# Kernel tuning notes

Measured on AMD Instinct MI355X. Metric: run time of the kernel, lower is better.

## Reference

```python
import jax, jax.numpy as jnp
import numpy as np

B, C, H, W = 8, 256, 64, 64
CQK = C // 8  # 32


def setup_inputs() -> dict:
    key = jax.random.key(0)
    ks = jax.random.split(key, 7)
    s = 0.02
    return {
        "feat_map": jax.random.normal(ks[0], (B, C, H, W), dtype=jnp.float32),
        "w1": jax.random.normal(ks[1], (CQK, C), dtype=jnp.float32) * s,
        "b1": jnp.zeros((CQK,), dtype=jnp.float32),
        "w2": jax.random.normal(ks[2], (CQK, C), dtype=jnp.float32) * s,
        "b2": jnp.zeros((CQK,), dtype=jnp.float32),
        "w3": jax.random.normal(ks[3], (C, C), dtype=jnp.float32) * s,
        "b3": jnp.zeros((C,), dtype=jnp.float32),
        "gamma": jnp.zeros((1,), dtype=jnp.float32),
    }


def reference(feat_map, w1, b1, w2, b2, w3, b3, gamma):
    b, c, h, w = feat_map.shape
    n = h * w
    x = feat_map.reshape(b, c, n)  # [B, C, N]
    # 1x1 convs == per-pixel linear maps over channels
    q = jnp.einsum("oc,bcn->bno", w1, x) + b1  # [B, N, C//8]
    k = jnp.einsum("oc,bcn->bon", w2, x) + b2[None, :, None]  # [B, C//8, N]
    v = jnp.einsum("oc,bcn->bon", w3, x) + b3[None, :, None]  # [B, C, N]
    relation = jnp.einsum("bno,bom->bnm", q, k)  # [B, N, N]
    attn = jax.nn.softmax(relation, axis=-1)  # softmax over last dim
    # feat_refine = bmm(v, attn^T): out[:, :, i] = sum_j v[:, :, j] * attn[i, j]
    feat_refine = jnp.einsum("bcm,bnm->bcn", v, attn).reshape(b, c, h, w)
    scaled = gamma[0] * feat_refine
    return (feat_refine, scaled)
```

## Files before the change

kernel.cpp:

```cpp
#include <hip/hip_runtime.h>
#include <cmath>

#define NB 8
#define CC 256
#define NPIX 4096
#define QB 128
#define KVB 64
#define NT (NPIX / KVB)
#define LOG2E 1.4426950408889634f

typedef __attribute__((ext_vector_type(4))) float f32x4;
typedef __attribute__((ext_vector_type(16))) float f32x16;
typedef __attribute__((ext_vector_type(8))) short s16x8;
typedef __attribute__((ext_vector_type(4))) unsigned int u32x4;
typedef __attribute__((ext_vector_type(2))) unsigned int u32x2;

__device__ __forceinline__ unsigned short f2bf(float f) {
    union { float f; unsigned int u; } v; v.f = f;
    return (unsigned short)((v.u + 0x7FFFu + ((v.u >> 16) & 1u)) >> 16);
}

__device__ __forceinline__ unsigned int cvt_pk_bf16(float lo, float hi) {
    unsigned int r;
    asm("v_cvt_pk_bf16_f32 %0, %1, %2" : "=v"(r) : "v"(lo), "v"(hi));
    return r;
}

__device__ __forceinline__ float u2f(unsigned int u) {
    union { unsigned int u; float f; } v; v.u = u; return v.f;
}

__global__ __launch_bounds__(320) void proj_gemm_kernel(
    const float* __restrict__ x,
    const float* __restrict__ w1, const float* __restrict__ b1,
    const float* __restrict__ w2, const float* __restrict__ b2,
    const float* __restrict__ w3, const float* __restrict__ b3,
    unsigned short* __restrict__ Qm, unsigned short* __restrict__ Km,
    unsigned short* __restrict__ Vm)
{
    const int b  = blockIdx.x >> 6;
    const int n0 = (blockIdx.x & 63) * 64;
    const int wave = threadIdx.x >> 6;
    const int lane = threadIdx.x & 63;
    const int cl = lane & 15, g = lane >> 4;

    const float* arow[4];
#pragma unroll
    for (int ct = 0; ct < 4; ++ct) {
        const int row = wave * 64 + ct * 16 + cl;
        if (row < 32)       arow[ct] = w1 + (size_t)row * 256;
        else if (row < 64)  arow[ct] = w2 + (size_t)(row - 32) * 256;
        else                arow[ct] = w3 + (size_t)(row - 64) * 256;
    }

    const float* xb = x + (size_t)b * CC * NPIX + n0 + cl;

    f32x4 acc[4][4];
#pragma unroll
    for (int ct = 0; ct < 4; ++ct)
#pragma unroll
        for (int nt = 0; nt < 4; ++nt) acc[ct][nt] = (f32x4){0.f, 0.f, 0.f, 0.f};

    for (int ks = 0; ks < 8; ++ks) {
        const int c0 = ks * 32;
        s16x8 ah[4];
#pragma unroll
        for (int ct = 0; ct < 4; ++ct) {
            const float* ap = arow[ct] + c0 + g * 8;
            f32x4 a0 = *(const f32x4*)ap;
            f32x4 a1 = *(const f32x4*)(ap + 4);
            u32x4 u;
            u[0] = cvt_pk_bf16(a0[0], a0[1]); u[1] = cvt_pk_bf16(a0[2], a0[3]);
            u[2] = cvt_pk_bf16(a1[0], a1[1]); u[3] = cvt_pk_bf16(a1[2], a1[3]);
            ah[ct] = __builtin_bit_cast(s16x8, u);
        }
#pragma unroll
        for (int nt = 0; nt < 4; ++nt) {
            const float* xp = xb + (size_t)(c0 + g * 8) * NPIX + nt * 16;
            float xe[8];
#pragma unroll
            for (int e = 0; e < 8; ++e) xe[e] = xp[(size_t)e * NPIX];
            u32x4 uh, ul;
#pragma unroll
            for (int p = 0; p < 4; ++p) {
                const unsigned int hp = cvt_pk_bf16(xe[2 * p], xe[2 * p + 1]);
                const float h0 = u2f(hp << 16);
                const float h1 = u2f(hp & 0xffff0000u);
                uh[p] = hp;
                ul[p] = cvt_pk_bf16(xe[2 * p] - h0, xe[2 * p + 1] - h1);
            }
            const s16x8 bh = __builtin_bit_cast(s16x8, uh);
            const s16x8 bl = __builtin_bit_cast(s16x8, ul);
#pragma unroll
            for (int ct = 0; ct < 4; ++ct)
                acc[ct][nt] = __builtin_amdgcn_mfma_f32_16x16x32_bf16(ah[ct], bh, acc[ct][nt], 0, 0, 0);
#pragma unroll
            for (int ct = 0; ct < 4; ++ct)
                acc[ct][nt] = __builtin_amdgcn_mfma_f32_16x16x32_bf16(ah[ct], bl, acc[ct][nt], 0, 0, 0);
        }
    }

    if (wave == 0) {
#pragma unroll
        for (int ct = 0; ct < 4; ++ct) {
#pragma unroll
            for (int nt = 0; nt < 4; ++nt) {
                const int n = n0 + nt * 16 + cl;
                const int co = ct * 16 + g * 4;
                f32x4 v = acc[ct][nt];
                if (ct < 2) {
                    const float q0 = (v[0] + b1[co + 0]) * LOG2E;
                    const float q1 = (v[1] + b1[co + 1]) * LOG2E;
                    const float q2 = (v[2] + b1[co + 2]) * LOG2E;
                    const float q3 = (v[3] + b1[co + 3]) * LOG2E;
                    u32x2 dd = {cvt_pk_bf16(q0, q1), cvt_pk_bf16(q2, q3)};
                    *(u32x2*)(Qm + ((size_t)b * NPIX + n) * 32 + co) = dd;
                } else {
                    const int ko = co - 32;
                    const float k0 = v[0] + b2[ko + 0];
                    const float k1 = v[1] + b2[ko + 1];
                    const float k2 = v[2] + b2[ko + 2];
                    const float k3 = v[3] + b2[ko + 3];
                    u32x2 dd = {cvt_pk_bf16(k0, k1), cvt_pk_bf16(k2, k3)};
                    *(u32x2*)(Km + ((size_t)b * NPIX + n) * 32 + ko) = dd;
                }
            }
        }
    } else {
        const int cvb = (wave - 1) * 64;
#pragma unroll
        for (int ct = 0; ct < 4; ++ct) {
#pragma unroll
            for (int nt = 0; nt < 4; ++nt) {
                const int n = n0 + nt * 16 + cl;
                const int cv = cvb + ct * 16 + g * 4;
#pragma unroll
                for (int r = 0; r < 4; ++r)
                    Vm[((size_t)b * CC + cv + r) * NPIX + n] = f2bf(acc[ct][nt][r] + b3[cv + r]);
            }
        }
    }
}

__global__ __launch_bounds__(256, 2) void attn_kernel(
    const unsigned short* __restrict__ Qm, const unsigned short* __restrict__ Km,
    const unsigned short* __restrict__ Vm, const float* __restrict__ gamma,
    float* __restrict__ out)
{
    __shared__ unsigned short Vs[2][CC * KVB];

    const int bid = ((blockIdx.x & 7) << 5) + (blockIdx.x >> 3);
    const int b = bid >> 5;
    const int q0 = (bid & 31) * QB;

    const int t = threadIdx.x;
    const int wave = t >> 6;
    const int lane = t & 63;
    const int q_ = lane & 31;
    const int hi = lane >> 5;

    const int qrow = q0 + wave * 32 + q_;

    s16x8 qf[2];
#pragma unroll
    for (int kh = 0; kh < 2; ++kh)
        qf[kh] = *(const s16x8*)(Qm + ((size_t)b * NPIX + qrow) * 32 + kh * 16 + hi * 8);

    f32x16 acc[8];
#pragma unroll
    for (int ct = 0; ct < 8; ++ct) acc[ct] = (f32x16){};

    float mrun = -__builtin_inff();
    float lrun = 0.f;

    const unsigned short* Kg = Km + (size_t)b * NPIX * 32;
    const unsigned short* Vg = Vm + (size_t)b * CC * NPIX;

    const int vr0 = t >> 3;
    const int cg = (t & 7) ^ (vr0 & 7);
    const unsigned short* vsrc = Vg + (size_t)vr0 * NPIX + cg * 8;

#define STAGE_V(tile, buf_)                                                    \
    {                                                                          \
        const int mm_ = (tile) * KVB;                                          \
        _Pragma("unroll")                                                      \
        for (int i_ = 0; i_ < 8; ++i_)                                         \
            __builtin_amdgcn_global_load_lds(                                  \
                (const __attribute__((address_space(1))) void*)(vsrc + (size_t)i_ * 32 * NPIX + mm_), \
                (__attribute__((address_space(3))) void*)(&Vs[buf_][i_ * 2048 + t * 8]), \
                16, 0, 0);                                                     \
    }

    s16x8 kf[2][2];
#define LOAD_KF(mm_)                                                           \
    {                                                                          \
        _Pragma("unroll")                                                      \
        for (int mt_ = 0; mt_ < 2; ++mt_)                                      \
            _Pragma("unroll")                                                  \
            for (int kh_ = 0; kh_ < 2; ++kh_)                                  \
                kf[mt_][kh_] = *(const s16x8*)(Kg + (size_t)((mm_) + 32 * mt_ + q_) * 32 + kh_ * 16 + hi * 8); \
    }

    STAGE_V(0, 0)
    LOAD_KF(0)

    int cur = 0;
    for (int it = 0; it < NT; ++it) {
        __syncthreads();

        if (it < NT - 1) STAGE_V(it + 1, cur ^ 1)

        f32x16 z = (f32x16){};
        f32x16 s0 = __builtin_amdgcn_mfma_f32_32x32x16_bf16(kf[0][0], qf[0], z, 0, 0, 0);
        s0 = __builtin_amdgcn_mfma_f32_32x32x16_bf16(kf[0][1], qf[1], s0, 0, 0, 0);
        f32x16 s1 = __builtin_amdgcn_mfma_f32_32x32x16_bf16(kf[1][0], qf[0], z, 0, 0, 0);
        s1 = __builtin_amdgcn_mfma_f32_32x32x16_bf16(kf[1][1], qf[1], s1, 0, 0, 0);

        LOAD_KF((((it + 1) & (NT - 1))) * KVB)

        float ml = -__builtin_inff();
#pragma unroll
        for (int r = 0; r < 16; ++r) ml = fmaxf(ml, s0[r]);
#pragma unroll
        for (int r = 0; r < 16; ++r) ml = fmaxf(ml, s1[r]);

        if (!__all(ml <= mrun + 8.f)) {
            ml = fmaxf(ml, __shfl_xor(ml, 32, 64));
            const float mnew = fmaxf(mrun, ml);
            const float alpha = __builtin_amdgcn_exp2f(mrun - mnew);
            mrun = mnew;
            lrun *= alpha;
#pragma unroll
            for (int ct = 0; ct < 8; ++ct) acc[ct] *= alpha;
        }

#pragma unroll
        for (int r = 0; r < 16; ++r) { s0[r] = __builtin_amdgcn_exp2f(s0[r] - mrun); lrun += s0[r]; }
#pragma unroll
        for (int r = 0; r < 16; ++r) { s1[r] = __builtin_amdgcn_exp2f(s1[r] - mrun); lrun += s1[r]; }

        unsigned int w0[4][2], w1[4][2];
#pragma unroll
        for (int s = 0; s < 4; ++s) {
            w0[s][0] = cvt_pk_bf16(s0[4 * s + 0], s0[4 * s + 1]);
            w0[s][1] = cvt_pk_bf16(s0[4 * s + 2], s0[4 * s + 3]);
            w1[s][0] = cvt_pk_bf16(s1[4 * s + 0], s1[4 * s + 1]);
            w1[s][1] = cvt_pk_bf16(s1[4 * s + 2], s1[4 * s + 3]);
        }

#pragma unroll
        for (int t4 = 0; t4 < 4; ++t4) {
            const int lt = t4 & 1;
            unsigned int a0 = (t4 < 2) ? w0[2 * lt][0] : w1[2 * lt][0];
            unsigned int b0 = (t4 < 2) ? w0[2 * lt + 1][0] : w1[2 * lt + 1][0];
            unsigned int a1 = (t4 < 2) ? w0[2 * lt][1] : w1[2 * lt][1];
            unsigned int b1 = (t4 < 2) ? w0[2 * lt + 1][1] : w1[2 * lt + 1][1];
            asm("v_permlane32_swap_b32 %0, %1" : "+v"(a0), "+v"(b0));
            asm("v_permlane32_swap_b32 %0, %1" : "+v"(a1), "+v"(b1));
            u32x4 bw = {a0, a1, b0, b1};
            const s16x8 pb = __builtin_bit_cast(s16x8, bw);

            __builtin_amdgcn_s_setprio(1);
#pragma unroll
            for (int ct = 0; ct < 8; ++ct) {
                const int c = 32 * ct + q_;
                const int slot = (2 * t4 + hi) ^ (c & 7);
                const s16x8 av = *(const s16x8*)(&Vs[cur][c * 64 + slot * 8]);
                acc[ct] = __builtin_amdgcn_mfma_f32_32x32x16_bf16(av, pb, acc[ct], 0, 0, 0);
            }
            __builtin_amdgcn_s_setprio(0);
        }

        cur ^= 1;
    }

    lrun += __shfl_xor(lrun, 32, 64);
    const float inv = 1.f / lrun;
    const float gm = gamma[0];
    float* out2 = out + (size_t)NB * CC * NPIX;
    const int n = qrow;
#pragma unroll
    for (int ct = 0; ct < 8; ++ct) {
#pragma unroll
        for (int r = 0; r < 16; ++r) {
            const int c = 32 * ct + (r & 3) + 8 * (r >> 2) + 4 * hi;
            const float val = acc[ct][r] * inv;
            const size_t idx = ((size_t)b * CC + c) * NPIX + n;
            out[idx] = val;
            out2[idx] = gm * val;
        }
    }
}

extern "C" void kernel_launch(void* const* d_in, const int* in_sizes, int n_in,
                              void* d_out, int out_size, void* d_ws, size_t ws_size,
                              hipStream_t stream) {
    (void)in_sizes; (void)n_in; (void)out_size; (void)ws_size;
    const float* x     = (const float*)d_in[0];
    const float* w1    = (const float*)d_in[1];
    const float* b1    = (const float*)d_in[2];
    const float* w2    = (const float*)d_in[3];
    const float* b2    = (const float*)d_in[4];
    const float* w3    = (const float*)d_in[5];
    const float* b3    = (const float*)d_in[6];
    const float* gamma = (const float*)d_in[7];
    float* out = (float*)d_out;

    unsigned short* Qm = (unsigned short*)d_ws;
    unsigned short* Km = Qm + (size_t)NB * NPIX * 32;
    unsigned short* Vm = Km + (size_t)NB * NPIX * 32;

    proj_gemm_kernel<<<NB * 64, 320, 0, stream>>>(x, w1, b1, w2, b2, w3, b3, Qm, Km, Vm);
    attn_kernel<<<NB * 32, 256, 0, stream>>>(Qm, Km, Vm, gamma, out);
}
```

Before: 135.7 us.

## Split KV range across two wave groups per block and merge softmax partials

Doubles the attention block to 512 threads, with two groups of four waves each processing half of the key/value sequence using separate double-buffered V tiles in LDS. At the end, per-row max and sum are exchanged via shared memory and the second group's rescaled accumulators are staged through LDS to be combined by the first group. This aims to raise waves per CU and latency hiding, since the grid has only one block per CU. The cost is doubled LDS usage and an extra merge phase with barriers.

Measured after the change: 124.6 us. 1.09x faster.

```diff
diff --git a/kernel.cpp b/kernel.cpp
--- a/kernel.cpp
+++ b/kernel.cpp
@@ -6,7 +6,7 @@
 #define NPIX 4096
 #define QB 128
 #define KVB 64
-#define NT (NPIX / KVB)
+#define NT2 32
 #define LOG2E 1.4426950408889634f
 
 typedef __attribute__((ext_vector_type(4))) float f32x4;
@@ -142,12 +142,14 @@
     }
 }
 
-__global__ __launch_bounds__(256, 2) void attn_kernel(
+__global__ __launch_bounds__(512, 2) void attn_kernel(
     const unsigned short* __restrict__ Qm, const unsigned short* __restrict__ Km,
     const unsigned short* __restrict__ Vm, const float* __restrict__ gamma,
     float* __restrict__ out)
 {
-    __shared__ unsigned short Vs[2][CC * KVB];
+    __shared__ unsigned short Vs[2][2][CC * KVB];
+    __shared__ float mArr[2][4][32];
+    __shared__ float lArr[2][4][32];
 
     const int bid = ((blockIdx.x & 7) << 5) + (blockIdx.x >> 3);
     const int b = bid >> 5;
@@ -158,8 +160,10 @@
     const int lane = t & 63;
     const int q_ = lane & 31;
     const int hi = lane >> 5;
-
-    const int qrow = q0 + wave * 32 + q_;
+    const int s = wave & 3;
+    const int h = wave >> 2;
+
+    const int qrow = q0 + s * 32 + q_;
 
     s16x8 qf[2];
 #pragma unroll
@@ -176,18 +180,19 @@
     const unsigned short* Kg = Km + (size_t)b * NPIX * 32;
     const unsigned short* Vg = Vm + (size_t)b * CC * NPIX;
 
-    const int vr0 = t >> 3;
-    const int cg = (t & 7) ^ (vr0 & 7);
+    const int tg = t & 255;
+    const int vr0 = tg >> 3;
+    const int cg = (tg & 7) ^ (vr0 & 7);
     const unsigned short* vsrc = Vg + (size_t)vr0 * NPIX + cg * 8;
 
 #define STAGE_V(tile, buf_)                                                    \
     {                                                                          \
-        const int mm_ = (tile) * KVB;                                          \
+        const int mm_ = h * 2048 + (tile) * KVB;                               \
         _Pragma("unroll")                                                      \
         for (int i_ = 0; i_ < 8; ++i_)                                         \
             __builtin_amdgcn_global_load_lds(                                  \
                 (const __attribute__((address_space(1))) void*)(vsrc + (size_t)i_ * 32 * NPIX + mm_), \
-                (__attribute__((address_space(3))) void*)(&Vs[buf_][i_ * 2048 + t * 8]), \
+                (__attribute__((address_space(3))) void*)(&Vs[h][buf_][i_ * 2048 + tg * 8]), \
                 16, 0, 0);                                                     \
     }
 
@@ -202,13 +207,13 @@
     }
 
     STAGE_V(0, 0)
-    LOAD_KF(0)
+    LOAD_KF(h * 2048)
 
     int cur = 0;
-    for (int it = 0; it < NT; ++it) {
+    for (int it = 0; it < NT2; ++it) {
         __syncthreads();
 
-        if (it < NT - 1) STAGE_V(it + 1, cur ^ 1)
+        if (it < NT2 - 1) STAGE_V(it + 1, cur ^ 1)
 
         f32x16 z = (f32x16){};
         f32x16 s0 = __builtin_amdgcn_mfma_f32_32x32x16_bf16(kf[0][0], qf[0], z, 0, 0, 0);
@@ -216,7 +221,7 @@
         f32x16 s1 = __builtin_amdgcn_mfma_f32_32x32x16_bf16(kf[1][0], qf[0], z, 0, 0, 0);
         s1 = __builtin_amdgcn_mfma_f32_32x32x16_bf16(kf[1][1], qf[1], s1, 0, 0, 0);
 
-        LOAD_KF((((it + 1) & (NT - 1))) * KVB)
+        LOAD_KF(h * 2048 + (((it + 1) & (NT2 - 1))) * KVB)
 
         float ml = -__builtin_inff();
 #pragma unroll
@@ -241,11 +246,11 @@
 
         unsigned int w0[4][2], w1[4][2];
 #pragma unroll
-        for (int s = 0; s < 4; ++s) {
-            w0[s][0] = cvt_pk_bf16(s0[4 * s + 0], s0[4 * s + 1]);
-            w0[s][1] = cvt_pk_bf16(s0[4 * s + 2], s0[4 * s + 3]);
-            w1[s][0] = cvt_pk_bf16(s1[4 * s + 0], s1[4 * s + 1]);
-            w1[s][1] = cvt_pk_bf16(s1[4 * s + 2], s1[4 * s + 3]);
+        for (int p = 0; p < 4; ++p) {
+            w0[p][0] = cvt_pk_bf16(s0[4 * p + 0], s0[4 * p + 1]);
+            w0[p][1] = cvt_pk_bf16(s0[4 * p + 2], s0[4 * p + 3]);
+            w1[p][0] = cvt_pk_bf16(s1[4 * p + 0], s1[4 * p + 1]);
+            w1[p][1] = cvt_pk_bf16(s1[4 * p + 2], s1[4 * p + 3]);
         }
 
 #pragma unroll
@@ -265,7 +270,7 @@
             for (int ct = 0; ct < 8; ++ct) {
                 const int c = 32 * ct + q_;
                 const int slot = (2 * t4 + hi) ^ (c & 7);
-                const s16x8 av = *(const s16x8*)(&Vs[cur][c * 64 + slot * 8]);
+                const s16x8 av = *(const s16x8*)(&Vs[h][cur][c * 64 + slot * 8]);
                 acc[ct] = __builtin_amdgcn_mfma_f32_32x32x16_bf16(av, pb, acc[ct], 0, 0, 0);
             }
             __builtin_amdgcn_s_setprio(0);
@@ -275,19 +280,43 @@
     }
 
     lrun += __shfl_xor(lrun, 32, 64);
-    const float inv = 1.f / lrun;
-    const float gm = gamma[0];
-    float* out2 = out + (size_t)NB * CC * NPIX;
-    const int n = qrow;
-#pragma unroll
-    for (int ct = 0; ct < 8; ++ct) {
-#pragma unroll
-        for (int r = 0; r < 16; ++r) {
-            const int c = 32 * ct + (r & 3) + 8 * (r >> 2) + 4 * hi;
-            const float val = acc[ct][r] * inv;
-            const size_t idx = ((size_t)b * CC + c) * NPIX + n;
-            out[idx] = val;
-            out2[idx] = gm * val;
+
+    __syncthreads();
+
+    if (lane < 32) { mArr[h][s][lane] = mrun; lArr[h][s][lane] = lrun; }
+    __syncthreads();
+
+    const float m_o = mArr[h ^ 1][s][q_];
+    const float l_o = lArr[h ^ 1][s][q_];
+    const float M = fmaxf(mrun, m_o);
+    const float f = __builtin_amdgcn_exp2f(mrun - M);
+    const float l_tot = lrun * f + l_o * __builtin_amdgcn_exp2f(m_o - M);
+
+    float* S = (float*)&Vs[0][0][0];
+    if (h == 1) {
+#pragma unroll
+        for (int ct = 0; ct < 8; ++ct)
+#pragma unroll
+            for (int r = 0; r < 16; ++r)
+                S[(ct * 16 + r) * 256 + s * 64 + lane] = acc[ct][r] * f;
+    }
+    __syncthreads();
+
+    if (h == 0) {
+        const float inv = 1.f / l_tot;
+        const float gm = gamma[0];
+        float* out2 = out + (size_t)NB * CC * NPIX;
+        const int n = qrow;
+#pragma unroll
+        for (int ct = 0; ct < 8; ++ct) {
+#pragma unroll
+            for (int r = 0; r < 16; ++r) {
+                const int c = 32 * ct + (r & 3) + 8 * (r >> 2) + 4 * hi;
+                const float val = (acc[ct][r] * f + S[(ct * 16 + r) * 256 + s * 64 + lane]) * inv;
+                const size_t idx = ((size_t)b * CC + c) * NPIX + n;
+                out[idx] = val;
+                out2[idx] = gm * val;
+            }
         }
     }
 }
@@ -311,5 +340,5 @@
     unsigned short* Vm = Km + (size_t)NB * NPIX * 32;
 
     proj_gemm_kernel<<<NB * 64, 320, 0, stream>>>(x, w1, b1, w2, b2, w3, b3, Qm, Km, Vm);
-    attn_kernel<<<NB * 32, 256, 0, stream>>>(Qm, Km, Vm, gamma, out);
-}
+    attn_kernel<<<NB * 32, 512, 0, stream>>>(Qm, Km, Vm, gamma, out);
+}
```
